# Kernel tuning notes

Hardware: AMD Instinct MI355X
Metric: run time of the kernel (lower is better)

Reference implementation:

```python
import jax, jax.numpy as jnp
import numpy as np

B = 64
H = W = 16
DIMS = [2048, 1024, 512, 256, 128, 1]


def setup_inputs() -> dict:
    key = jax.random.key(0)
    ks = jax.random.split(key, 11)
    inp = {"x": jax.random.normal(ks[0], (B, DIMS[0], H, W), dtype=jnp.float32)}
    for i in range(5):
        fan_in = DIMS[i]
        out = DIMS[i + 1]
        # per-sample weights [B, out, in, 1, 1], scaled ~1/sqrt(fan_in) to keep sigmoids unsaturated
        inp[f"fc{i+1}w"] = jax.random.normal(ks[1 + 2 * i], (B, out, fan_in, 1, 1), dtype=jnp.float32) / jnp.sqrt(jnp.float32(fan_in))
        inp[f"fc{i+1}b"] = jax.random.normal(ks[2 + 2 * i], (B, out), dtype=jnp.float32) * 0.1
    return inp


def _target_fc(h, w, b):
    # grouped 1x1 conv with groups=B == per-sample linear over channel dim
    # h: [B, in, H, W], w: [B, out, in, 1, 1], b: [B, out] -> [B, out, H, W]
    return jnp.einsum("boi,bihw->bohw", w[..., 0, 0], h) + b[:, :, None, None]


def reference(x, fc1w, fc1b, fc2w, fc2b, fc3w, fc3b, fc4w, fc4b, fc5w, fc5b):
    q = jax.nn.sigmoid(_target_fc(x, fc1w, fc1b))
    q = jax.nn.sigmoid(_target_fc(q, fc2w, fc2b))
    q = jax.nn.sigmoid(_target_fc(q, fc3w, fc3b))
    q = jax.nn.sigmoid(_target_fc(q, fc4w, fc4b))
    q = _target_fc(q, fc5w, fc5b)  # [B, 1, H, W]
    q = jnp.squeeze(q, axis=1)      # .squeeze() -> [B, H, W]
    return jax.nn.sigmoid(q)
```

## Files before the change

### kernel.cpp

```cpp
#include <hip/hip_runtime.h>
#include <hip/hip_bf16.h>
#include <hip/hip_fp16.h>


typedef __attribute__((ext_vector_type(4)))  float    f32x4;
typedef __attribute__((ext_vector_type(16))) float    f32x16;
typedef __attribute__((ext_vector_type(8)))  short    short8;
typedef __attribute__((ext_vector_type(4)))  short    short4v;
typedef __attribute__((ext_vector_type(8)))  _Float16 half8;

__device__ __forceinline__ unsigned short f2h_bits(float f) {
  return __builtin_bit_cast(unsigned short, (_Float16)f);
}
__device__ __forceinline__ float h2f(short h) {
  return (float)__builtin_bit_cast(_Float16, (unsigned short)h);
}

__global__ __launch_bounds__(256) void transpose_cvt(const float* __restrict__ X,
                                                     short* __restrict__ XT) {
  __shared__ float tile[32][33];
  const int b  = blockIdx.z;
  const int c0 = blockIdx.x * 32, s0 = blockIdx.y * 32;
  const int tl = threadIdx.x & 31, tw = threadIdx.x >> 5;
  const float* xp = X + ((size_t)b * 2048 + c0) * 256 + s0;
#pragma unroll
  for (int i = 0; i < 4; ++i) {
    const int c = tw * 4 + i;
    tile[c][tl] = xp[(size_t)c * 256 + tl];
  }
  __syncthreads();
  short* op = XT + ((size_t)(b * 256 + s0)) * 2048 + c0;
#pragma unroll
  for (int i = 0; i < 4; ++i) {
    const int s = tw * 4 + i;
    op[(size_t)s * 2048 + tl] = (short)f2h_bits(tile[tl][s]);
  }
}

struct WFrag { f32x4 a0, a1, b0, b1; };

template <int M, int K, int WAVES, int NSPLIT>
__global__ __launch_bounds__(WAVES * 64, 2) void gemm_layer(
    const float* __restrict__ W, const float* __restrict__ bias,
    const short* __restrict__ Xin, short* __restrict__ Out) {
  constexpr int BK    = 32;
  constexpr int NT    = K / BK;
  constexpr int NCG   = 8 / NSPLIT;
  constexpr int TILES = NCG * 2;
  constexpr int BM    = WAVES * 32;
  constexpr int MT    = M / BM;
  constexpr int TPW   = TILES / WAVES;
  constexpr int NS    = 256 / NSPLIT;

  __shared__ __align__(16) short lds[2][TILES * 512];

  const int tid = threadIdx.x;
  const int w = tid >> 6, l = tid & 63;
  const int lr = l & 31;
  const int lh = l >> 5;

  const int per_b = MT * NSPLIT;
  const int b   = blockIdx.x / per_b;
  const int rem = blockIdx.x % per_b;
  const int mt  = rem / NSPLIT;
  const int ns  = rem % NSPLIT;
  const int m0  = mt * BM + w * 32;

  const float* Wb = W + ((size_t)b * M + m0) * K;
  const short* Xb = Xin + (size_t)b * 256 * K + (size_t)ns * NS * K;

  f32x16 acc[NCG] = {};

  auto stage = [&](int buf, int t) {
    const int k0 = t * BK;
#pragma unroll
    for (int i = 0; i < TPW; ++i) {
      const int T  = w * TPW + i;
      const int s  = ((T >> 1) << 5) + lr;
      const int kk = ((T & 1) << 4) + (lh << 3);
      const short* src = Xb + (size_t)s * K + k0 + kk;
      __builtin_amdgcn_global_load_lds(
          (const __attribute__((address_space(1))) void*)src,
          (__attribute__((address_space(3))) void*)&lds[buf][T * 512],
          16, 0, 0);
    }
  };

  const float* wrow = Wb + (size_t)lr * K + (lh << 3);
  auto load_wfrag = [&](int t) {
    const float* wp = wrow + t * BK;
    WFrag f;
    f.a0 = *(const f32x4*)wp;        f.a1 = *(const f32x4*)(wp + 4);
    f.b0 = *(const f32x4*)(wp + 16); f.b1 = *(const f32x4*)(wp + 20);
    return f;
  };

  WFrag wc = load_wfrag(0);
  stage(0, 0);
  __syncthreads();

  int cur = 0;
  for (int t = 0; t < NT; ++t) {
    if (t + 1 < NT) stage(cur ^ 1, t + 1);
    WFrag wn;
    if (t + 1 < NT) wn = load_wfrag(t + 1);
    {
      half8 af;
#pragma unroll
      for (int j = 0; j < 4; ++j) { af[j] = (_Float16)wc.a0[j]; af[j + 4] = (_Float16)wc.a1[j]; }
#pragma unroll
      for (int cg = 0; cg < NCG; ++cg) {
        const short8 braw = *(const short8*)&lds[cur][(cg * 2 + 0) * 512 + l * 8];
        acc[cg] = __builtin_amdgcn_mfma_f32_32x32x16_f16(af, __builtin_bit_cast(half8, braw),
                                                         acc[cg], 0, 0, 0);
      }
    }
    {
      half8 af;
#pragma unroll
      for (int j = 0; j < 4; ++j) { af[j] = (_Float16)wc.b0[j]; af[j + 4] = (_Float16)wc.b1[j]; }
#pragma unroll
      for (int cg = 0; cg < NCG; ++cg) {
        const short8 braw = *(const short8*)&lds[cur][(cg * 2 + 1) * 512 + l * 8];
        acc[cg] = __builtin_amdgcn_mfma_f32_32x32x16_f16(af, __builtin_bit_cast(half8, braw),
                                                         acc[cg], 0, 0, 0);
      }
    }
    __syncthreads();
    if (t + 1 < NT) wc = wn;
    cur ^= 1;
  }

  float brow[16];
#pragma unroll
  for (int r = 0; r < 16; ++r) {
    const int row = (r & 3) + 8 * (r >> 2) + (lh << 2);
    brow[r] = bias[(size_t)b * M + m0 + row];
  }
#pragma unroll
  for (int cg = 0; cg < NCG; ++cg) {
    const int s = ns * NS + cg * 32 + lr;
    short* op = Out + ((size_t)b * 256 + s) * M + m0;
#pragma unroll
    for (int rg = 0; rg < 4; ++rg) {
      short4v pk;
#pragma unroll
      for (int j = 0; j < 4; ++j) {
        const int r = rg * 4 + j;
        float v = acc[cg][r] + brow[r];
        v = 1.0f / (1.0f + __expf(-v));
        pk[j] = (short)f2h_bits(v);
      }
      *(short4v*)(op + rg * 8 + (lh << 2)) = pk;
    }
  }
}

__global__ __launch_bounds__(256) void fc5_sig(const float* __restrict__ W5,
                                               const float* __restrict__ B5,
                                               const short* __restrict__ H4,
                                               float* __restrict__ out) {
  const int tid = blockIdx.x * 256 + threadIdx.x;
  const int oi = tid >> 3;
  const int r  = tid & 7;
  const int b  = oi >> 8;
  const short* hp = H4 + ((size_t)oi << 7) + r * 16;
  const float* wp = W5 + b * 128 + r * 16;
  const short8 hh0 = *(const short8*)hp;
  const short8 hh1 = *(const short8*)(hp + 8);
  const f32x4 w0 = *(const f32x4*)wp;
  const f32x4 w1 = *(const f32x4*)(wp + 4);
  const f32x4 w2 = *(const f32x4*)(wp + 8);
  const f32x4 w3 = *(const f32x4*)(wp + 12);
  float a = 0.f;
#pragma unroll
  for (int j = 0; j < 4; ++j) a += h2f(hh0[j]) * w0[j];
#pragma unroll
  for (int j = 0; j < 4; ++j) a += h2f(hh0[j + 4]) * w1[j];
#pragma unroll
  for (int j = 0; j < 4; ++j) a += h2f(hh1[j]) * w2[j];
#pragma unroll
  for (int j = 0; j < 4; ++j) a += h2f(hh1[j + 4]) * w3[j];
  a += __shfl_xor(a, 1);
  a += __shfl_xor(a, 2);
  a += __shfl_xor(a, 4);
  if (r == 0) out[oi] = 1.0f / (1.0f + __expf(-(a + B5[b])));
}

extern "C" void kernel_launch(void* const* d_in, const int* in_sizes, int n_in,
                              void* d_out, int out_size, void* d_ws, size_t ws_size,
                              hipStream_t stream) {
  const float* x  = (const float*)d_in[0];
  const float* w1 = (const float*)d_in[1];  const float* b1 = (const float*)d_in[2];
  const float* w2 = (const float*)d_in[3];  const float* b2 = (const float*)d_in[4];
  const float* w3 = (const float*)d_in[5];  const float* b3 = (const float*)d_in[6];
  const float* w4 = (const float*)d_in[7];  const float* b4 = (const float*)d_in[8];
  const float* w5 = (const float*)d_in[9];  const float* b5 = (const float*)d_in[10];

  char* ws = (char*)d_ws;
  short* bufA = (short*)ws;
  short* bufB = (short*)(ws + (size_t)67108864);
  float* out  = (float*)d_out;

  transpose_cvt<<<dim3(64, 8, 64), 256, 0, stream>>>(x, bufA);
  gemm_layer<1024, 2048, 4, 1><<<512, 256, 0, stream>>>(w1, b1, bufA, bufB);
  gemm_layer<512, 1024, 2, 1><<<512, 128, 0, stream>>>(w2, b2, bufB, bufA);
  gemm_layer<256, 512, 2, 2><<<512, 128, 0, stream>>>(w3, b3, bufA, bufB);
  gemm_layer<128, 256, 1, 2><<<512, 64, 0, stream>>>(w4, b4, bufB, bufA);
  fc5_sig<<<512, 256, 0, stream>>>(w5, b5, bufA, out);
}
```

Before: 377.5 us.

## Double K tile depth and stage epilogue through LDS for coalesced stores

Raises the GEMM K-step from 32 to 64, so each iteration issues twice the MFMAs between barriers and halves the number of synchronisations and loop overheads. The output epilogue now writes each wave's fp16 results into a small per-wave LDS scratch, then reads them back so each lane stores two contiguous 16-byte chunks instead of scattered 8-byte writes. This costs more LDS and registers per block, which could lower occupancy.

```diff
diff --git a/kernel.cpp b/kernel.cpp
--- a/kernel.cpp
+++ b/kernel.cpp
@@ -37,22 +37,25 @@
   }
 }
 
-struct WFrag { f32x4 a0, a1, b0, b1; };
+struct WFrag { f32x4 v[8]; };
 
 template <int M, int K, int WAVES, int NSPLIT>
 __global__ __launch_bounds__(WAVES * 64, 2) void gemm_layer(
     const float* __restrict__ W, const float* __restrict__ bias,
     const short* __restrict__ Xin, short* __restrict__ Out) {
-  constexpr int BK    = 32;
+  constexpr int BK    = 64;
+  constexpr int KH    = BK / 16;
   constexpr int NT    = K / BK;
   constexpr int NCG   = 8 / NSPLIT;
-  constexpr int TILES = NCG * 2;
+  constexpr int TILES = NCG * KH;
   constexpr int BM    = WAVES * 32;
   constexpr int MT    = M / BM;
   constexpr int TPW   = TILES / WAVES;
   constexpr int NS    = 256 / NSPLIT;
+  constexpr int EPIW  = 40;
 
   __shared__ __align__(16) short lds[2][TILES * 512];
+  __shared__ __align__(16) short epi[WAVES][32][EPIW];
 
   const int tid = threadIdx.x;
   const int w = tid >> 6, l = tid & 63;
@@ -76,8 +79,8 @@
 #pragma unroll
     for (int i = 0; i < TPW; ++i) {
       const int T  = w * TPW + i;
-      const int s  = ((T >> 1) << 5) + lr;
-      const int kk = ((T & 1) << 4) + (lh << 3);
+      const int s  = (T / KH) * 32 + lr;
+      const int kk = (T % KH) * 16 + (lh << 3);
       const short* src = Xb + (size_t)s * K + k0 + kk;
       __builtin_amdgcn_global_load_lds(
           (const __attribute__((address_space(1))) void*)src,
@@ -88,10 +91,13 @@
 
   const float* wrow = Wb + (size_t)lr * K + (lh << 3);
   auto load_wfrag = [&](int t) {
-    const float* wp = wrow + t * BK;
     WFrag f;
-    f.a0 = *(const f32x4*)wp;        f.a1 = *(const f32x4*)(wp + 4);
-    f.b0 = *(const f32x4*)(wp + 16); f.b1 = *(const f32x4*)(wp + 20);
+#pragma unroll
+    for (int h = 0; h < KH; ++h) {
+      const float* wp = wrow + t * BK + h * 16;
+      f.v[2 * h]     = *(const f32x4*)wp;
+      f.v[2 * h + 1] = *(const f32x4*)(wp + 4);
+    }
     return f;
   };
 
@@ -101,31 +107,24 @@
 
   int cur = 0;
   for (int t = 0; t < NT; ++t) {
-    if (t + 1 < NT) stage(cur ^ 1, t + 1);
     WFrag wn;
     if (t + 1 < NT) wn = load_wfrag(t + 1);
-    {
+    if (t + 1 < NT) stage(cur ^ 1, t + 1);
+#pragma unroll
+    for (int h = 0; h < KH; ++h) {
       half8 af;
 #pragma unroll
-      for (int j = 0; j < 4; ++j) { af[j] = (_Float16)wc.a0[j]; af[j + 4] = (_Float16)wc.a1[j]; }
+      for (int j = 0; j < 4; ++j) {
+        af[j]     = (_Float16)wc.v[2 * h][j];
+        af[j + 4] = (_Float16)wc.v[2 * h + 1][j];
+      }
 #pragma unroll
       for (int cg = 0; cg < NCG; ++cg) {
-        const short8 braw = *(const short8*)&lds[cur][(cg * 2 + 0) * 512 + l * 8];
+        const short8 braw = *(const short8*)&lds[cur][(cg * KH + h) * 512 + l * 8];
         acc[cg] = __builtin_amdgcn_mfma_f32_32x32x16_f16(af, __builtin_bit_cast(half8, braw),
                                                          acc[cg], 0, 0, 0);
       }
     }
-    {
-      half8 af;
-#pragma unroll
-      for (int j = 0; j < 4; ++j) { af[j] = (_Float16)wc.b0[j]; af[j + 4] = (_Float16)wc.b1[j]; }
-#pragma unroll
-      for (int cg = 0; cg < NCG; ++cg) {
-        const short8 braw = *(const short8*)&lds[cur][(cg * 2 + 1) * 512 + l * 8];
-        acc[cg] = __builtin_amdgcn_mfma_f32_32x32x16_f16(af, __builtin_bit_cast(half8, braw),
-                                                         acc[cg], 0, 0, 0);
-      }
-    }
     __syncthreads();
     if (t + 1 < NT) wc = wn;
     cur ^= 1;
@@ -137,10 +136,9 @@
     const int row = (r & 3) + 8 * (r >> 2) + (lh << 2);
     brow[r] = bias[(size_t)b * M + m0 + row];
   }
+  const int s_loc = l >> 1, hi = l & 1;
 #pragma unroll
   for (int cg = 0; cg < NCG; ++cg) {
-    const int s = ns * NS + cg * 32 + lr;
-    short* op = Out + ((size_t)b * 256 + s) * M + m0;
 #pragma unroll
     for (int rg = 0; rg < 4; ++rg) {
       short4v pk;
@@ -151,8 +149,13 @@
         v = 1.0f / (1.0f + __expf(-v));
         pk[j] = (short)f2h_bits(v);
       }
-      *(short4v*)(op + rg * 8 + (lh << 2)) = pk;
-    }
+      *(short4v*)&epi[w][lr][rg * 8 + (lh << 2)] = pk;
+    }
+    const short8 r0 = *(const short8*)&epi[w][s_loc][hi * 16];
+    const short8 r1 = *(const short8*)&epi[w][s_loc][hi * 16 + 8];
+    short* op = Out + ((size_t)b * 256 + ns * NS + cg * 32 + s_loc) * M + m0 + hi * 16;
+    *(short8*)op       = r0;
+    *(short8*)(op + 8) = r1;
   }
 }
 
```

Result: faster. 345.0 us (-8.6%).
